# Kernel optimization log

Measured on AMD Instinct MI355X. Metric: run time of the kernel, lower is better.

## Reference

```python
import jax, jax.numpy as jnp
import numpy as np

DEPTH = 8
INPUT_WIDTH = 64
INNER_WIDTH = 32
BATCH = 65536
N_NODES = 2 ** DEPTH - 1   # 255 inner nodes
N_LEAVES = 2 ** DEPTH      # 256 bins
EPS = 1e-8


def _tree_paths(depth):
    """For each leaf, the inner-node index at each level and whether the path
    goes right (right child uses 1 - decision, mirroring hstack([p, 1-p]) indexing)."""
    node_idx = np.zeros((2 ** depth, depth), dtype=np.int32)
    is_right = np.zeros((2 ** depth, depth), dtype=bool)
    for leaf in range(2 ** depth):
        idx = 0
        for level in range(depth):
            bit = (leaf >> (depth - 1 - level)) & 1
            node_idx[leaf, level] = idx
            is_right[leaf, level] = bool(bit)
            idx = 2 * idx + 1 + bit
    return node_idx, is_right

_NODE_IDX_NP, _IS_RIGHT_NP = _tree_paths(DEPTH)
NODE_IDX = jnp.asarray(_NODE_IDX_NP)   # [L, depth]
IS_RIGHT = jnp.asarray(_IS_RIGHT_NP)   # [L, depth]


def _init_b_i():
    """Replicates PartialRadialLayer.init_tree_weights: thresholds evenly dividing [0,1],
    stored as logits so sigmoid(b_i) recovers the threshold."""
    b = np.zeros(N_NODES, dtype=np.float64)
    b[0] = -0.5
    used = 1
    for i in range(1, DEPTH):
        n_nodes = 2 ** i
        div = float(2 ** (i + 1))
        for node in range(n_nodes):
            b[used + node] = -(2 * node + 1) / div
        used += n_nodes
    return np.log(-b / (1.0 + b)).astype(np.float32).reshape(1, -1)


def setup_inputs() -> dict:
    key = jax.random.key(0)
    kx, kr, kt = jax.random.split(key, 3)
    x = jax.random.normal(kx, (BATCH, INPUT_WIDTH), dtype=jnp.float32)
    # kaiming_normal_ on [1, input_width]: fan_in = input_width
    ray = jax.random.normal(kr, (1, INPUT_WIDTH), dtype=jnp.float32) * np.sqrt(2.0 / INPUT_WIDTH)
    # kaiming_normal_ on [L, I, W]: fan_in = I * W
    inner_transforms = jax.random.normal(kt, (N_LEAVES, INPUT_WIDTH, INNER_WIDTH), dtype=jnp.float32) * np.sqrt(2.0 / (INPUT_WIDTH * INNER_WIDTH))
    w_i = jnp.zeros((1, N_NODES), dtype=jnp.float32)
    a_i = 5.0 * jnp.ones((1, N_NODES), dtype=jnp.float32)
    b_i = jnp.asarray(_init_b_i())
    return {"x": x, "ray": ray, "inner_transforms": inner_transforms,
            "w_i": w_i, "b_i": b_i, "a_i": a_i}


def reference(x, ray, inner_transforms, w_i, b_i, a_i):
    # angles: arccos(cosine_similarity(x, ray)) / pi
    x_norm = jnp.maximum(jnp.linalg.norm(x, axis=1), EPS)            # [B]
    r_norm = jnp.maximum(jnp.linalg.norm(ray, axis=1), EPS)          # [1]
    cos = jnp.clip((x @ ray[0]) / (x_norm * r_norm), -1.0, 1.0)      # [B]
    angles = jnp.arccos(cos) / jnp.pi                                # [B]

    # per-node decisions
    node_fns = (0.5 + jax.nn.sigmoid(w_i)) * angles[:, None] - jax.nn.sigmoid(b_i)  # [B, N]
    decisions = jax.nn.sigmoid(node_fns * (1.0 + a_i))                               # [B, N]

    # soft bin distribution: product along each root-to-leaf path
    g = decisions[:, NODE_IDX]                       # [B, L, depth]
    vals = jnp.where(IS_RIGHT, 1.0 - g, g)           # right child -> 1 - p
    distribution = jnp.prod(vals, axis=2)            # [B, L]

    # weighted per-leaf transforms: einsum('bi,liw->blw') then ('bl,blo->bo'), fused
    out = jnp.einsum('bl,bi,liw->bw', distribution, x, inner_transforms)
    return out
```

## Files before the change

### kernel.cpp

```cpp
#include <hip/hip_runtime.h>
#include <hip/hip_bf16.h>

#define NLEAF 256
#define MBLK 128
#define THREADS 512

typedef __attribute__((ext_vector_type(4))) float f32x4;
typedef __attribute__((ext_vector_type(4))) unsigned int uint4v;
typedef __attribute__((ext_vector_type(8))) __bf16 bf16x8;
typedef __attribute__((ext_vector_type(4))) __bf16 bf16x4;

#define OFF_DIST 0
#define OFF_T    65536
#define OFF_AC   73728
#define OFF_BC   74752
#define OFF_ANG  75776
#define OFF_RAY  76288
#define SMEM_BYTES 76544

__device__ __forceinline__ float sigf(float s) { return 1.0f / (1.0f + __expf(-s)); }

__device__ __forceinline__ int permr(int r) {
  return (r & 0x63) | ((r & 0x0C) << 1) | ((r & 0x10) >> 2);
}

__global__ __launch_bounds__(256) void prep_T(const float* __restrict__ T,
                                              __bf16* __restrict__ wsT) {
  __shared__ char tile[4096];
  const int l = blockIdx.x;
  const float* src = T + (size_t)l * 2048;
  const int t = threadIdx.x;
#pragma unroll
  for (int p = 0; p < 2; ++p) {
    int e = p * 1024 + t * 4;
    f32x4 v = *(const f32x4*)(src + e);
    int k = e >> 5, w0 = e & 31;
#pragma unroll
    for (int j = 0; j < 4; ++j) {
      int w = w0 + j;
      int off = (w * 128 + 2 * k) ^ ((w & 7) << 4);
      *(__bf16*)(tile + off) = (__bf16)v[j];
    }
  }
  __syncthreads();
  *(uint4v*)((char*)wsT + (size_t)l * 4096 + t * 16) = *(const uint4v*)(tile + t * 16);
}

template <bool USE_WS>
__global__ __launch_bounds__(THREADS, 4)
void prl_main(const float* __restrict__ x, const float* __restrict__ ray,
              const float* __restrict__ w_i, const float* __restrict__ b_i,
              const float* __restrict__ a_i, const void* __restrict__ tsrc,
              float* __restrict__ out) {
  extern __shared__ char smem[];
  const int tid = threadIdx.x;
  const int lane = tid & 63;
  const int wid = tid >> 6;
  const int rg = wid >> 1;
  const int cg = wid & 1;
  const int g = lane >> 4;
  const int ln = lane & 15;
  const int row0 = blockIdx.x * MBLK;

  float* A_c = (float*)(smem + OFF_AC);
  float* B_c = (float*)(smem + OFF_BC);
  float* angles = (float*)(smem + OFF_ANG);
  float* ray_l = (float*)(smem + OFF_RAY);
  __bf16* distb = (__bf16*)(smem + OFF_DIST);

  if (tid < 255) {
    float aa = 1.0f + a_i[tid];
    A_c[tid] = (0.5f + sigf(w_i[tid])) * aa;
    B_c[tid] = -sigf(b_i[tid]) * aa;
  }
  if (tid >= 256 && tid < 320) ray_l[tid - 256] = ray[tid - 256];
  __syncthreads();

  float* xp = (float*)(smem + OFF_DIST);
  {
    const float* xg = x + (size_t)row0 * 64;
#pragma unroll
    for (int p = 0; p < 4; ++p) {
      int idx = p * 512 + tid;
      f32x4 v = *(const f32x4*)(xg + idx * 4);
      *(f32x4*)(xp + idx * 4) = v;
      int cgr = idx & 15;
      f32x4 rv = *(const f32x4*)(ray_l + cgr * 4);
      float a0 = v[0] * v[0] + v[1] * v[1] + v[2] * v[2] + v[3] * v[3];
      float a1 = v[0] * rv[0] + v[1] * rv[1] + v[2] * rv[2] + v[3] * rv[3];
      float a2 = rv[0] * rv[0] + rv[1] * rv[1] + rv[2] * rv[2] + rv[3] * rv[3];
#pragma unroll
      for (int s = 1; s < 16; s <<= 1) {
        a0 += __shfl_xor(a0, s, 64);
        a1 += __shfl_xor(a1, s, 64);
        a2 += __shfl_xor(a2, s, 64);
      }
      if ((tid & 15) == 0) {
        int r = idx >> 4;
        float xn = fmaxf(sqrtf(a0), 1e-8f);
        float rn = fmaxf(sqrtf(a2), 1e-8f);
        float cs = a1 / (xn * rn);
        cs = fminf(fmaxf(cs, -1.0f), 1.0f);
        angles[r] = acosf(cs) * 0.31830988618379067f;
      }
    }
  }
  __syncthreads();

  bf16x8 afrag[2][2];
#pragma unroll
  for (int mt = 0; mt < 2; ++mt)
#pragma unroll
    for (int kt = 0; kt < 2; ++kt) {
      int rl = rg * 32 + mt * 16 + ln;
      int k0 = kt * 32 + g * 8;
      f32x4 u0 = *(const f32x4*)(xp + rl * 64 + k0);
      f32x4 u1 = *(const f32x4*)(xp + rl * 64 + k0 + 4);
      bf16x8 af;
      af[0] = (__bf16)u0[0]; af[1] = (__bf16)u0[1];
      af[2] = (__bf16)u0[2]; af[3] = (__bf16)u0[3];
      af[4] = (__bf16)u1[0]; af[5] = (__bf16)u1[1];
      af[6] = (__bf16)u1[2]; af[7] = (__bf16)u1[3];
      afrag[mt][kt] = af;
    }
  __syncthreads();

  __bf16* PA = (__bf16*)(smem + OFF_T);
  __bf16* PB = (__bf16*)(smem + OFF_T + 4096);
  if (tid < 128) {
    float ang = angles[tid];
    float d = sigf(fmaf(A_c[0], ang, B_c[0]));
    PA[tid] = (__bf16)d;
    PA[128 + tid] = (__bf16)(1.0f - d);
  }
  __syncthreads();
  if (tid < 256) {
    int n = tid >> 7, r = tid & 127;
    float p = (float)PA[tid];
    float ang = angles[r];
    float d = sigf(fmaf(A_c[1 + n], ang, B_c[1 + n]));
    PB[(2 * n) * 128 + r] = (__bf16)(p * d);
    PB[(2 * n + 1) * 128 + r] = (__bf16)(p * (1.0f - d));
  }
  __syncthreads();
  {
    int n = tid >> 7, r = tid & 127;
    float p = (float)PB[tid];
    float ang = angles[r];
    float d = sigf(fmaf(A_c[3 + n], ang, B_c[3 + n]));
    PA[(2 * n) * 128 + r] = (__bf16)(p * d);
    PA[(2 * n + 1) * 128 + r] = (__bf16)(p * (1.0f - d));
  }
  __syncthreads();
#pragma unroll
  for (int it = 0; it < 2; ++it) {
    int e = it * 512 + tid;
    int n = e >> 7, r = e & 127;
    float p = (float)PA[e];
    float ang = angles[r];
    float d = sigf(fmaf(A_c[7 + n], ang, B_c[7 + n]));
    PB[(2 * n) * 128 + r] = (__bf16)(p * d);
    PB[(2 * n + 1) * 128 + r] = (__bf16)(p * (1.0f - d));
  }
  __syncthreads();
  {
    const int r = tid & 127;
    const int pr = permr(r);
    const float ang = angles[r];
#pragma unroll
    for (int it = 0; it < 4; ++it) {
      int n4 = it * 4 + (tid >> 7);
      float p4 = (float)PB[n4 * 128 + r];
      float d4 = sigf(fmaf(A_c[15 + n4], ang, B_c[15 + n4]));
      float p5[2] = {p4 * d4, p4 * (1.0f - d4)};
#pragma unroll
      for (int b5 = 0; b5 < 2; ++b5) {
        int n5 = 2 * n4 + b5;
        float d5 = sigf(fmaf(A_c[31 + n5], ang, B_c[31 + n5]));
        float p6[2] = {p5[b5] * d5, p5[b5] * (1.0f - d5)};
#pragma unroll
        for (int b6 = 0; b6 < 2; ++b6) {
          int n6 = 2 * n5 + b6;
          float d6 = sigf(fmaf(A_c[63 + n6], ang, B_c[63 + n6]));
          float p7[2] = {p6[b6] * d6, p6[b6] * (1.0f - d6)};
#pragma unroll
          for (int b7 = 0; b7 < 2; ++b7) {
            int n7 = 2 * n6 + b7;
            float d7 = sigf(fmaf(A_c[127 + n7], ang, B_c[127 + n7]));
            float pv = p7[b7];
            distb[(2 * n7) * 128 + pr] = (__bf16)(pv * d7);
            distb[(2 * n7 + 1) * 128 + pr] = (__bf16)(pv * (1.0f - d7));
          }
        }
      }
    }
  }

  f32x4 acc0 = {}, acc1 = {};
  const int wB = cg * 16 + ln;
  const int ad0 = (wB * 128 + g * 16) ^ ((wB & 7) << 4);
  const int ad1 = (wB * 128 + 64 + g * 16) ^ ((wB & 7) << 4);
  char* tb = smem + OFF_T;

  uint4v tv = {};
  if constexpr (USE_WS) {
    if (tid < 256) {
      tv = *(const uint4v*)((const char*)tsrc + tid * 16);
    }
  }
  __syncthreads();
  if constexpr (USE_WS) {
    if (tid < 256) {
      *(uint4v*)(tb + tid * 16) = tv;
      tv = *(const uint4v*)((const char*)tsrc + 4096 + tid * 16);
    }
  }
  __syncthreads();

  const f32x4 zero = {0.0f, 0.0f, 0.0f, 0.0f};
  for (int l = 0; l < NLEAF; ++l) {
    char* cur = tb + (l & 1) * 4096;
    char* nxt = tb + ((l + 1) & 1) * 4096;
    if constexpr (USE_WS) {
      if (tid < 256) {
        if (l + 1 < NLEAF) *(uint4v*)(nxt + tid * 16) = tv;
        if (l + 2 < NLEAF)
          tv = *(const uint4v*)((const char*)tsrc + (size_t)(l + 2) * 4096 + tid * 16);
      }
    }
    bf16x8 q = *(const bf16x8*)(distb + l * 128 + rg * 32 + g * 8);
    f32x4 dv0 = (f32x4){(float)q[0], (float)q[1], (float)q[2], (float)q[3]};
    f32x4 dv1 = (f32x4){(float)q[4], (float)q[5], (float)q[6], (float)q[7]};
    bf16x8 b0, b1;
    if constexpr (USE_WS) {
      b0 = *(const bf16x8*)(cur + ad0);
      b1 = *(const bf16x8*)(cur + ad1);
    } else {
      const float* tp0 = (const float*)tsrc + (size_t)l * 2048 + (g * 8) * 32 + wB;
      const float* tp1 = tp0 + 32 * 32;
#pragma unroll
      for (int j = 0; j < 8; ++j) {
        b0[j] = (__bf16)tp0[j * 32];
        b1[j] = (__bf16)tp1[j * 32];
      }
    }
    f32x4 y0 = __builtin_amdgcn_mfma_f32_16x16x32_bf16(afrag[0][0], b0, zero, 0, 0, 0);
    y0 = __builtin_amdgcn_mfma_f32_16x16x32_bf16(afrag[0][1], b1, y0, 0, 0, 0);
    f32x4 y1 = __builtin_amdgcn_mfma_f32_16x16x32_bf16(afrag[1][0], b0, zero, 0, 0, 0);
    y1 = __builtin_amdgcn_mfma_f32_16x16x32_bf16(afrag[1][1], b1, y1, 0, 0, 0);
    acc0 += dv0 * y0;
    acc1 += dv1 * y1;
    if constexpr (USE_WS) __syncthreads();
  }

#pragma unroll
  for (int e = 0; e < 4; ++e) {
    int row = row0 + rg * 32 + g * 4 + e;
    out[(size_t)row * 32 + cg * 16 + ln] = acc0[e];
    out[(size_t)(row + 16) * 32 + cg * 16 + ln] = acc1[e];
  }
}

extern "C" void kernel_launch(void* const* d_in, const int* in_sizes, int n_in,
                              void* d_out, int out_size, void* d_ws, size_t ws_size,
                              hipStream_t stream) {
  const float* x = (const float*)d_in[0];
  const float* ray = (const float*)d_in[1];
  const float* T = (const float*)d_in[2];
  const float* w_i = (const float*)d_in[3];
  const float* b_i = (const float*)d_in[4];
  const float* a_i = (const float*)d_in[5];
  float* out = (float*)d_out;

  const int nblk = 65536 / MBLK;
  bool use_ws = ws_size >= (size_t)NLEAF * 4096;
  if (use_ws) {
    hipFuncSetAttribute(reinterpret_cast<const void*>(&prl_main<true>),
                        hipFuncAttributeMaxDynamicSharedMemorySize, SMEM_BYTES);
    prep_T<<<256, 256, 0, stream>>>(T, (__bf16*)d_ws);
    prl_main<true><<<nblk, THREADS, SMEM_BYTES, stream>>>(x, ray, w_i, b_i, a_i, d_ws, out);
  } else {
    hipFuncSetAttribute(reinterpret_cast<const void*>(&prl_main<false>),
                        hipFuncAttributeMaxDynamicSharedMemorySize, SMEM_BYTES);
    prl_main<false><<<nblk, THREADS, SMEM_BYTES, stream>>>(x, ray, w_i, b_i, a_i, T, out);
  }
}
```

Before: 165.3 us.

## Load pre-laid-out bf16 transform fragments directly from global into registers

The prep kernel now writes each leaf's bf16 transform in an MFMA-fragment-ready order, so every lane can load its B operands with two contiguous 16-byte global loads. The main loop drops the LDS double buffer and its per-leaf __syncthreads. Instead it keeps a four-deep register prefetch ring that is unrolled by four leaves. This removes one block-wide barrier per leaf and the LDS staging traffic. In exchange, all warps re-read the transform from L2/global and register pressure rises.

```diff
diff --git a/kernel.cpp b/kernel.cpp
--- a/kernel.cpp
+++ b/kernel.cpp
@@ -38,7 +38,8 @@
 #pragma unroll
     for (int j = 0; j < 4; ++j) {
       int w = w0 + j;
-      int off = (w * 128 + 2 * k) ^ ((w & 7) << 4);
+      int off = (w >> 4) * 2048 + (k >> 5) * 1024 +
+                (((k >> 3) & 3) * 16 + (w & 15)) * 16 + (k & 7) * 2;
       *(__bf16*)(tile + off) = (__bf16)v[j];
     }
   }
@@ -195,63 +196,73 @@
       }
     }
   }
+  __syncthreads();
 
   f32x4 acc0 = {}, acc1 = {};
-  const int wB = cg * 16 + ln;
-  const int ad0 = (wB * 128 + g * 16) ^ ((wB & 7) << 4);
-  const int ad1 = (wB * 128 + 64 + g * 16) ^ ((wB & 7) << 4);
-  char* tb = smem + OFF_T;
-
-  uint4v tv = {};
+  const f32x4 zero = {0.0f, 0.0f, 0.0f, 0.0f};
+  const __bf16* dbase = distb + rg * 32 + g * 8;
+
+#define COMPUTE(B0, B1, L)                                                         \
+  {                                                                                \
+    bf16x8 q = *(const bf16x8*)(dbase + (L) * 128);                                \
+    f32x4 dv0 = (f32x4){(float)q[0], (float)q[1], (float)q[2], (float)q[3]};       \
+    f32x4 dv1 = (f32x4){(float)q[4], (float)q[5], (float)q[6], (float)q[7]};       \
+    f32x4 y0 = __builtin_amdgcn_mfma_f32_16x16x32_bf16(afrag[0][0], B0, zero, 0, 0, 0); \
+    y0 = __builtin_amdgcn_mfma_f32_16x16x32_bf16(afrag[0][1], B1, y0, 0, 0, 0);    \
+    f32x4 y1 = __builtin_amdgcn_mfma_f32_16x16x32_bf16(afrag[1][0], B0, zero, 0, 0, 0); \
+    y1 = __builtin_amdgcn_mfma_f32_16x16x32_bf16(afrag[1][1], B1, y1, 0, 0, 0);    \
+    acc0 += dv0 * y0;                                                              \
+    acc1 += dv1 * y1;                                                              \
+  }
+
   if constexpr (USE_WS) {
-    if (tid < 256) {
-      tv = *(const uint4v*)((const char*)tsrc + tid * 16);
-    }
-  }
-  __syncthreads();
-  if constexpr (USE_WS) {
-    if (tid < 256) {
-      *(uint4v*)(tb + tid * 16) = tv;
-      tv = *(const uint4v*)((const char*)tsrc + 4096 + tid * 16);
-    }
-  }
-  __syncthreads();
-
-  const f32x4 zero = {0.0f, 0.0f, 0.0f, 0.0f};
-  for (int l = 0; l < NLEAF; ++l) {
-    char* cur = tb + (l & 1) * 4096;
-    char* nxt = tb + ((l + 1) & 1) * 4096;
-    if constexpr (USE_WS) {
-      if (tid < 256) {
-        if (l + 1 < NLEAF) *(uint4v*)(nxt + tid * 16) = tv;
-        if (l + 2 < NLEAF)
-          tv = *(const uint4v*)((const char*)tsrc + (size_t)(l + 2) * 4096 + tid * 16);
-      }
-    }
-    bf16x8 q = *(const bf16x8*)(distb + l * 128 + rg * 32 + g * 8);
-    f32x4 dv0 = (f32x4){(float)q[0], (float)q[1], (float)q[2], (float)q[3]};
-    f32x4 dv1 = (f32x4){(float)q[4], (float)q[5], (float)q[6], (float)q[7]};
-    bf16x8 b0, b1;
-    if constexpr (USE_WS) {
-      b0 = *(const bf16x8*)(cur + ad0);
-      b1 = *(const bf16x8*)(cur + ad1);
-    } else {
+    const char* bp = (const char*)tsrc + cg * 2048 + (size_t)lane * 16;
+    bf16x8 s0a, s0b, s1a, s1b, s2a, s2b, s3a, s3b;
+    s0a = *(const bf16x8*)(bp);
+    s0b = *(const bf16x8*)(bp + 1024);
+    s1a = *(const bf16x8*)(bp + 4096);
+    s1b = *(const bf16x8*)(bp + 4096 + 1024);
+    for (int l = 0; l < NLEAF; l += 4) {
+      {
+        const char* q = bp + (size_t)(l + 2) * 4096;
+        s2a = *(const bf16x8*)(q);
+        s2b = *(const bf16x8*)(q + 1024);
+      }
+      COMPUTE(s0a, s0b, l);
+      {
+        const char* q = bp + (size_t)(l + 3) * 4096;
+        s3a = *(const bf16x8*)(q);
+        s3b = *(const bf16x8*)(q + 1024);
+      }
+      COMPUTE(s1a, s1b, l + 1);
+      if (l + 4 < NLEAF) {
+        const char* q = bp + (size_t)(l + 4) * 4096;
+        s0a = *(const bf16x8*)(q);
+        s0b = *(const bf16x8*)(q + 1024);
+      }
+      COMPUTE(s2a, s2b, l + 2);
+      if (l + 5 < NLEAF) {
+        const char* q = bp + (size_t)(l + 5) * 4096;
+        s1a = *(const bf16x8*)(q);
+        s1b = *(const bf16x8*)(q + 1024);
+      }
+      COMPUTE(s3a, s3b, l + 3);
+    }
+  } else {
+    const int wB = cg * 16 + ln;
+    for (int l = 0; l < NLEAF; ++l) {
       const float* tp0 = (const float*)tsrc + (size_t)l * 2048 + (g * 8) * 32 + wB;
       const float* tp1 = tp0 + 32 * 32;
+      bf16x8 b0, b1;
 #pragma unroll
       for (int j = 0; j < 8; ++j) {
         b0[j] = (__bf16)tp0[j * 32];
         b1[j] = (__bf16)tp1[j * 32];
       }
-    }
-    f32x4 y0 = __builtin_amdgcn_mfma_f32_16x16x32_bf16(afrag[0][0], b0, zero, 0, 0, 0);
-    y0 = __builtin_amdgcn_mfma_f32_16x16x32_bf16(afrag[0][1], b1, y0, 0, 0, 0);
-    f32x4 y1 = __builtin_amdgcn_mfma_f32_16x16x32_bf16(afrag[1][0], b0, zero, 0, 0, 0);
-    y1 = __builtin_amdgcn_mfma_f32_16x16x32_bf16(afrag[1][1], b1, y1, 0, 0, 0);
-    acc0 += dv0 * y0;
-    acc1 += dv1 * y1;
-    if constexpr (USE_WS) __syncthreads();
-  }
+      COMPUTE(b0, b1, l);
+    }
+  }
+#undef COMPUTE
 
 #pragma unroll
   for (int e = 0; e < 4; ++e) {
```

Result: faster. 158.7 us (-4.0%).
